# Performance work log

Measured on AMD Instinct MI355X. Metric: run time of the kernel, lower is better.

## Reference

```python
import jax, jax.numpy as jnp
import numpy as np

HEADS = 16
DIM_HEAD = 64
SCALE = DIM_HEAD ** -0.5


def setup_inputs() -> dict:
    key = jax.random.key(0)
    ks = jax.random.split(key, 7)
    b, n, m, d = 2, 2048, 2048, 1024
    inner = HEADS * DIM_HEAD  # 1024
    patch_embed = jax.random.normal(ks[0], (b, n, d), dtype=jnp.float32)
    pixel_embed = jax.random.normal(ks[1], (b, m, d), dtype=jnp.float32)
    s = 1.0 / np.sqrt(d)
    Wq = jax.random.normal(ks[2], (d, inner), dtype=jnp.float32) * s
    Wk = jax.random.normal(ks[3], (d, inner), dtype=jnp.float32) * s
    Wv = jax.random.normal(ks[4], (d, inner), dtype=jnp.float32) * s
    Wo = jax.random.normal(ks[5], (inner, d), dtype=jnp.float32) * (1.0 / np.sqrt(inner))
    bo = jax.random.normal(ks[6], (d,), dtype=jnp.float32) * 0.01
    return {"patch_embed": patch_embed, "pixel_embed": pixel_embed,
            "Wq": Wq, "Wk": Wk, "Wv": Wv, "Wo": Wo, "bo": bo}


def reference(patch_embed, pixel_embed, Wq, Wk, Wv, Wo, bo):
    b, n, _ = patch_embed.shape
    h, dh = HEADS, DIM_HEAD
    # projections
    q = patch_embed @ Wq  # [b, n, h*dh]
    k = pixel_embed @ Wk  # [b, m, h*dh]
    v = pixel_embed @ Wv  # [b, m, h*dh]
    # split heads: [b, seq, h, dh]
    q = q.reshape(b, n, h, dh)
    k = k.reshape(b, -1, h, dh)
    v = v.reshape(b, -1, h, dh)
    sim = jnp.einsum('bihd,bjhd->bhij', q, k) * SCALE  # [b, h, n, m]
    attn = jax.nn.softmax(sim, axis=-1)
    out = jnp.einsum('bhij,bjhd->bihd', attn, v)  # [b, n, h, dh]
    out = out.reshape(b, n, h * dh)
    return out @ Wo + bo  # [b, n, query_dim]
```

## Files before the change

kernel.cpp:

```cpp
#include <hip/hip_runtime.h>

#define SEQ 2048
#define DMODEL 1024
#define HEADS 16
#define DH 64
#define QSCALE 0.180336880f

typedef __attribute__((ext_vector_type(8))) short short8;
typedef __attribute__((ext_vector_type(4))) float f32x4;

__device__ __forceinline__ ushort f2bf(float x) {
  union { float f; unsigned u; } v; v.f = x;
  return (ushort)((v.u + 0x7fffu + ((v.u >> 16) & 1u)) >> 16);
}

__device__ __forceinline__ void gld16(const ushort* g, ushort* l) {
  __builtin_amdgcn_global_load_lds(
      (const __attribute__((address_space(1))) unsigned int*)g,
      (__attribute__((address_space(3))) unsigned int*)l, 16, 0, 0);
}

__device__ __forceinline__ size_t qk_idx(int bh, int s, int d) {
  return ((((size_t)bh * (SEQ / 16) + (s >> 4)) * 2 + (d >> 5)) * 64 +
          ((d >> 3) & 3) * 16 + (s & 15)) * 8 + (d & 7);
}
__device__ __forceinline__ size_t v_idx(int bh, int s, int d) {
  return ((((size_t)bh * 4 + (d >> 4)) * (SEQ / 32) + (s >> 5)) * 64 +
          ((s >> 3) & 3) * 16 + (d & 15)) * 8 + (s & 7);
}

__global__ __launch_bounds__(256) void prologue(
    const float* __restrict__ patch, const float* __restrict__ pixel,
    const float* __restrict__ W0, const float* __restrict__ W1,
    const float* __restrict__ W2, const float* __restrict__ W3,
    ushort* __restrict__ pb, ushort* __restrict__ xb,
    ushort* __restrict__ O0, ushort* __restrict__ O1,
    ushort* __restrict__ O2, ushort* __restrict__ O3) {
  const int z = blockIdx.z;
  const int tx = threadIdx.x, ty = threadIdx.y;
  if (z < 2) {
    const float4* in = (const float4*)(z ? pixel : patch);
    ushort4* out = (ushort4*)(z ? xb : pb);
    const int base = (blockIdx.y * 32 + blockIdx.x) * 256 + ty * 32 + tx;
#pragma unroll
    for (int rep = 0; rep < 4; ++rep) {
      const int i = base + rep * 262144;
      float4 f = in[i];
      out[i] = make_ushort4(f2bf(f.x), f2bf(f.y), f2bf(f.z), f2bf(f.w));
    }
    return;
  }
  __shared__ float tile[32][33];
  const int zz = z - 2;
  const float* in = zz == 0 ? W0 : zz == 1 ? W1 : zz == 2 ? W2 : W3;
  ushort* out = zz == 0 ? O0 : zz == 1 ? O1 : zz == 2 ? O2 : O3;
  const float scale = zz == 0 ? QSCALE : 1.0f;
  const int n0 = blockIdx.x * 32, k0 = blockIdx.y * 32;
#pragma unroll
  for (int i = 0; i < 4; ++i)
    tile[ty + i * 8][tx] = in[(size_t)(k0 + ty + i * 8) * DMODEL + n0 + tx];
  __syncthreads();
#pragma unroll
  for (int i = 0; i < 4; ++i)
    out[(size_t)(n0 + ty + i * 8) * DMODEL + k0 + tx] =
        f2bf(tile[tx][ty + i * 8] * scale);
}

__global__ __launch_bounds__(256) void mfma_gemm_qkv(
    const ushort* __restrict__ pb, const ushort* __restrict__ xb,
    const ushort* __restrict__ wqt, const ushort* __restrict__ wkt,
    const ushort* __restrict__ wvt, ushort* __restrict__ qws,
    ushort* __restrict__ kws, ushort* __restrict__ vws) {
  __shared__ __align__(16) ushort As[128 * 64];
  __shared__ __align__(16) ushort Bs[128 * 64];
  const int z = blockIdx.z;
  const ushort* A = (z == 0) ? pb : xb;
  const ushort* Bt = (z == 0) ? wqt : (z == 1) ? wkt : wvt;

  const int t = threadIdx.x;
  const int w = t >> 6, lane = t & 63, ln = lane & 15, q = lane >> 4;
  const int wm = w & 1, wn = w >> 1;
  const int row0 = blockIdx.y * 128, col0 = blockIdx.x * 128;
  const int sw = ln & 7;

  f32x4 acc[4][4];
#pragma unroll
  for (int i = 0; i < 4; ++i)
#pragma unroll
    for (int j = 0; j < 4; ++j) acc[i][j] = (f32x4){0.f, 0.f, 0.f, 0.f};

  for (int k0 = 0; k0 < DMODEL; k0 += 64) {
    __syncthreads();
#pragma unroll
    for (int rep = 0; rep < 4; ++rep) {
      const int u0 = rep * 256 + w * 64;
      const int u = u0 + lane;
      const int r = u >> 3, gl = (u & 7) ^ (r & 7);
      gld16(&A[(size_t)(row0 + r) * DMODEL + k0 + gl * 8], &As[u0 * 8]);
      gld16(&Bt[(size_t)(col0 + r) * DMODEL + k0 + gl * 8], &Bs[u0 * 8]);
    }
    __syncthreads();
#pragma unroll
    for (int ks = 0; ks < 2; ++ks) {
      short8 af[4], bf[4];
#pragma unroll
      for (int rt = 0; rt < 4; ++rt)
        af[rt] = *(const short8*)&As[(wm * 64 + rt * 16 + ln) * 64 +
                                     (((ks * 4 + q) ^ sw) * 8)];
#pragma unroll
      for (int ct = 0; ct < 4; ++ct)
        bf[ct] = *(const short8*)&Bs[(wn * 64 + ct * 16 + ln) * 64 +
                                     (((ks * 4 + q) ^ sw) * 8)];
#pragma unroll
      for (int rt = 0; rt < 4; ++rt)
#pragma unroll
        for (int ct = 0; ct < 4; ++ct)
          acc[rt][ct] = __builtin_amdgcn_mfma_f32_16x16x32_bf16(af[rt], bf[ct],
                                                                acc[rt][ct], 0, 0, 0);
    }
  }

  if (z < 2) {
    ushort* dst = z == 0 ? qws : kws;
#pragma unroll
    for (int rt = 0; rt < 4; ++rt)
#pragma unroll
      for (int ct = 0; ct < 4; ++ct) {
        const int c = col0 + wn * 64 + ct * 16 + ln;
        const int h = c >> 6, d = c & 63;
#pragma unroll
        for (int reg = 0; reg < 4; ++reg) {
          const int r = row0 + wm * 64 + rt * 16 + q * 4 + reg;
          const int b = r >> 11, s = r & (SEQ - 1);
          dst[qk_idx(b * HEADS + h, s, d)] = f2bf(acc[rt][ct][reg]);
        }
      }
  } else {
#pragma unroll
    for (int rt = 0; rt < 4; ++rt)
#pragma unroll
      for (int ct = 0; ct < 4; ++ct) {
        const int c = col0 + wn * 64 + ct * 16 + ln;
        const int h = c >> 6, d = c & 63;
        const int r0 = row0 + wm * 64 + rt * 16 + q * 4;
        const int b = r0 >> 11, s0 = r0 & (SEQ - 1);
        ushort4 u4 = make_ushort4(f2bf(acc[rt][ct][0]), f2bf(acc[rt][ct][1]),
                                  f2bf(acc[rt][ct][2]), f2bf(acc[rt][ct][3]));
        *(ushort4*)&vws[v_idx(b * HEADS + h, s0, d)] = u4;
      }
  }
}

__global__ __launch_bounds__(256, 3) void flash_mfma(
    const ushort* __restrict__ Qg, const ushort* __restrict__ Kg,
    const ushort* __restrict__ Vg, ushort* __restrict__ Og) {
  __shared__ __align__(16) ushort Kst[2][8 * 512];
  __shared__ __align__(16) ushort Vst[2][8 * 512];
  __shared__ __align__(16) ushort Ps[128 * 72];

  const int t = threadIdx.x;
  const int w = t >> 6, lane = t & 63, ln = lane & 15, q = lane >> 4;
  const int bh = blockIdx.x;
  const int qt = blockIdx.y;

  const ushort* qg = Qg + (size_t)bh * SEQ * DH;
  const ushort* kg = Kg + (size_t)bh * SEQ * DH;
  const ushort* vg = Vg + (size_t)bh * DH * SEQ;

  short8 qf[2][2];
#pragma unroll
  for (int rt = 0; rt < 2; ++rt)
#pragma unroll
    for (int ks = 0; ks < 2; ++ks)
      qf[rt][ks] = *(const short8*)
          &qg[(((size_t)(qt * 8 + w * 2 + rt) * 2 + ks) * 64 + lane) * 8];

  float l_i[2][4];
  f32x4 acc_o[2][4];
#pragma unroll
  for (int rt = 0; rt < 2; ++rt)
#pragma unroll
    for (int reg = 0; reg < 4; ++reg) l_i[rt][reg] = 0.f;
#pragma unroll
  for (int rt = 0; rt < 2; ++rt)
#pragma unroll
    for (int nt = 0; nt < 4; ++nt) acc_o[rt][nt] = (f32x4){0.f, 0.f, 0.f, 0.f};

#pragma unroll
  for (int i = 0; i < 4; ++i) {
    const int f = w * 4 + i;
    if (f < 8) {
      gld16(&kg[(size_t)(0 * 8 + f) * 512 + lane * 8], &Kst[0][f * 512]);
    } else {
      const int f2 = f - 8, nt = f2 >> 1, ks2 = f2 & 1;
      gld16(&vg[(size_t)(nt * (SEQ / 32) + 0 * 2 + ks2) * 512 + lane * 8],
            &Vst[0][f2 * 512]);
    }
  }
  __syncthreads();

  for (int kt = 0; kt < SEQ / 64; ++kt) {
    const int cur = kt & 1;
    if (kt + 1 < SEQ / 64) {
      const int nxt = cur ^ 1;
#pragma unroll
      for (int i = 0; i < 4; ++i) {
        const int f = w * 4 + i;
        if (f < 8) {
          gld16(&kg[(size_t)((kt + 1) * 8 + f) * 512 + lane * 8],
                &Kst[nxt][f * 512]);
        } else {
          const int f2 = f - 8, nt = f2 >> 1, ks2 = f2 & 1;
          gld16(&vg[(size_t)(nt * (SEQ / 32) + (kt + 1) * 2 + ks2) * 512 +
                    lane * 8],
                &Vst[nxt][f2 * 512]);
        }
      }
    }

    f32x4 accs[2][4];
#pragma unroll
    for (int rt = 0; rt < 2; ++rt)
#pragma unroll
      for (int ct = 0; ct < 4; ++ct) accs[rt][ct] = (f32x4){0.f, 0.f, 0.f, 0.f};
#pragma unroll
    for (int ks = 0; ks < 2; ++ks)
#pragma unroll
      for (int ct = 0; ct < 4; ++ct) {
        const short8 bf = *(const short8*)&Kst[cur][(ct * 2 + ks) * 512 + lane * 8];
#pragma unroll
        for (int rt = 0; rt < 2; ++rt)
          accs[rt][ct] = __builtin_amdgcn_mfma_f32_16x16x32_bf16(
              qf[rt][ks], bf, accs[rt][ct], 0, 0, 0);
      }

#pragma unroll
    for (int rt = 0; rt < 2; ++rt)
#pragma unroll
      for (int ct = 0; ct < 4; ++ct)
#pragma unroll
        for (int reg = 0; reg < 4; ++reg) {
          const float p = __builtin_amdgcn_exp2f(accs[rt][ct][reg]);
          l_i[rt][reg] += p;
          union { float f; unsigned u; } v; v.f = p;
          Ps[(w * 32 + rt * 16 + q * 4 + reg) * 72 + ct * 16 + ln] =
              (ushort)((v.u + 0x8000u) >> 16);
        }

#pragma unroll
    for (int ks2 = 0; ks2 < 2; ++ks2) {
      short8 pa[2];
#pragma unroll
      for (int rt = 0; rt < 2; ++rt)
        pa[rt] = *(const short8*)&Ps[(w * 32 + rt * 16 + ln) * 72 +
                                     ks2 * 32 + q * 8];
#pragma unroll
      for (int nt = 0; nt < 4; ++nt) {
        const short8 bv = *(const short8*)&Vst[cur][(nt * 2 + ks2) * 512 + lane * 8];
#pragma unroll
        for (int rt = 0; rt < 2; ++rt)
          acc_o[rt][nt] = __builtin_amdgcn_mfma_f32_16x16x32_bf16(
              pa[rt], bv, acc_o[rt][nt], 0, 0, 0);
      }
    }

    __syncthreads();
  }

  const int b = bh >> 4, h = bh & 15;
#pragma unroll
  for (int rt = 0; rt < 2; ++rt)
#pragma unroll
    for (int reg = 0; reg < 4; ++reg) {
      float l = l_i[rt][reg];
      l += __shfl_xor(l, 1, 16);
      l += __shfl_xor(l, 2, 16);
      l += __shfl_xor(l, 4, 16);
      l += __shfl_xor(l, 8, 16);
      const float inv = 1.0f / l;
      const int s = qt * 128 + w * 32 + rt * 16 + q * 4 + reg;
#pragma unroll
      for (int nt = 0; nt < 4; ++nt)
        Og[(size_t)(b * SEQ + s) * DMODEL + h * DH + nt * 16 + ln] =
            f2bf(acc_o[rt][nt][reg] * inv);
    }
}

__global__ __launch_bounds__(256) void mfma_gemm_out(const ushort* __restrict__ A,
                                                     const ushort* __restrict__ Bt,
                                                     const float* __restrict__ bias,
                                                     float* __restrict__ dst) {
  __shared__ __align__(16) ushort As[64 * 64];
  __shared__ __align__(16) ushort Bs[128 * 64];
  const int t = threadIdx.x;
  const int w = t >> 6, lane = t & 63, ln = lane & 15, q = lane >> 4;
  const int wm = w & 1, wn = w >> 1;
  const int row0 = blockIdx.y * 64, col0 = blockIdx.x * 128;
  const int sw = ln & 7;

  f32x4 acc[2][4];
#pragma unroll
  for (int i = 0; i < 2; ++i)
#pragma unroll
    for (int j = 0; j < 4; ++j) acc[i][j] = (f32x4){0.f, 0.f, 0.f, 0.f};

  for (int k0 = 0; k0 < DMODEL; k0 += 64) {
    __syncthreads();
#pragma unroll
    for (int rep = 0; rep < 2; ++rep) {
      const int u0 = rep * 256 + w * 64;
      const int u = u0 + lane;
      const int r = u >> 3, gl = (u & 7) ^ (r & 7);
      gld16(&A[(size_t)(row0 + r) * DMODEL + k0 + gl * 8], &As[u0 * 8]);
    }
#pragma unroll
    for (int rep = 0; rep < 4; ++rep) {
      const int u0 = rep * 256 + w * 64;
      const int u = u0 + lane;
      const int r = u >> 3, gl = (u & 7) ^ (r & 7);
      gld16(&Bt[(size_t)(col0 + r) * DMODEL + k0 + gl * 8], &Bs[u0 * 8]);
    }
    __syncthreads();
#pragma unroll
    for (int ks = 0; ks < 2; ++ks) {
      short8 af[2], bf[4];
#pragma unroll
      for (int rt = 0; rt < 2; ++rt)
        af[rt] = *(const short8*)&As[(wm * 32 + rt * 16 + ln) * 64 +
                                     (((ks * 4 + q) ^ sw) * 8)];
#pragma unroll
      for (int ct = 0; ct < 4; ++ct)
        bf[ct] = *(const short8*)&Bs[(wn * 64 + ct * 16 + ln) * 64 +
                                     (((ks * 4 + q) ^ sw) * 8)];
#pragma unroll
      for (int rt = 0; rt < 2; ++rt)
#pragma unroll
        for (int ct = 0; ct < 4; ++ct)
          acc[rt][ct] = __builtin_amdgcn_mfma_f32_16x16x32_bf16(af[rt], bf[ct],
                                                                acc[rt][ct], 0, 0, 0);
    }
  }

#pragma unroll
  for (int rt = 0; rt < 2; ++rt)
#pragma unroll
    for (int ct = 0; ct < 4; ++ct) {
      const int c = col0 + wn * 64 + ct * 16 + ln;
      const float bi = bias[c];
#pragma unroll
      for (int reg = 0; reg < 4; ++reg) {
        const int r = row0 + wm * 32 + rt * 16 + q * 4 + reg;
        dst[(size_t)r * DMODEL + c] = acc[rt][ct][reg] + bi;
      }
    }
}

extern "C" void kernel_launch(void* const* d_in, const int* in_sizes, int n_in,
                              void* d_out, int out_size, void* d_ws,
                              size_t ws_size, hipStream_t stream) {
  const float* patch = (const float*)d_in[0];
  const float* pixel = (const float*)d_in[1];
  const float* Wq = (const float*)d_in[2];
  const float* Wk = (const float*)d_in[3];
  const float* Wv = (const float*)d_in[4];
  const float* Wo = (const float*)d_in[5];
  const float* bo = (const float*)d_in[6];
  float* out = (float*)d_out;

  const size_t E = (size_t)2 * SEQ * DMODEL;
  const size_t W = (size_t)DMODEL * DMODEL;
  ushort* pb  = (ushort*)d_ws;
  ushort* xb  = pb + E;
  ushort* wqt = xb + E;
  ushort* wkt = wqt + W;
  ushort* wvt = wkt + W;
  ushort* wot = wvt + W;
  ushort* qws = wot + W;
  ushort* kws = qws + E;
  ushort* vws = kws + E;
  ushort* aws = vws + E;

  prologue<<<dim3(32, 32, 6), dim3(32, 8), 0, stream>>>(
      patch, pixel, Wq, Wk, Wv, Wo, pb, xb, wqt, wkt, wvt, wot);
  mfma_gemm_qkv<<<dim3(8, 32, 3), 256, 0, stream>>>(pb, xb, wqt, wkt, wvt,
                                                    qws, kws, vws);
  flash_mfma<<<dim3(32, 16), 256, 0, stream>>>(qws, kws, vws, aws);
  mfma_gemm_out<<<dim3(8, 64), 256, 0, stream>>>(aws, wot, bo, out);
}
```

Before: 195.9 us.

## Switch P and V to fp16 with packed conversion, merge K/V LDS buffers

Stores V and the softmax probabilities as fp16 using the packed cvt_pkrtz instruction in place of manual bf16 rounding, and runs the PV product with the f16 MFMA. K and V staging buffers are merged into one LDS array with precomputed source pointers and strides, which removes per-iteration index arithmetic. Occupancy hint lowered from 3 to 2 blocks per CU, allowing more registers per thread. fp16 gives more mantissa precision than bf16 but less range; the probabilities are at most about 1 and the V projections are moderate, so overflow is unlikely.

```diff
diff --git a/kernel.cpp b/kernel.cpp
--- a/kernel.cpp
+++ b/kernel.cpp
@@ -8,10 +8,18 @@
 
 typedef __attribute__((ext_vector_type(8))) short short8;
 typedef __attribute__((ext_vector_type(4))) float f32x4;
+typedef _Float16 half8 __attribute__((ext_vector_type(8)));
+typedef __fp16 fp16x2 __attribute__((ext_vector_type(2)));
 
 __device__ __forceinline__ ushort f2bf(float x) {
   union { float f; unsigned u; } v; v.f = x;
   return (ushort)((v.u + 0x7fffu + ((v.u >> 16) & 1u)) >> 16);
+}
+
+__device__ __forceinline__ ushort2 pk16(float x, float y) {
+  union { fp16x2 h; ushort2 u; } v;
+  v.h = __builtin_amdgcn_cvt_pkrtz(x, y);
+  return v.u;
 }
 
 __device__ __forceinline__ void gld16(const ushort* g, ushort* l) {
@@ -144,18 +152,18 @@
         const int h = c >> 6, d = c & 63;
         const int r0 = row0 + wm * 64 + rt * 16 + q * 4;
         const int b = r0 >> 11, s0 = r0 & (SEQ - 1);
-        ushort4 u4 = make_ushort4(f2bf(acc[rt][ct][0]), f2bf(acc[rt][ct][1]),
-                                  f2bf(acc[rt][ct][2]), f2bf(acc[rt][ct][3]));
-        *(ushort4*)&vws[v_idx(b * HEADS + h, s0, d)] = u4;
-      }
-  }
-}
-
-__global__ __launch_bounds__(256, 3) void flash_mfma(
+        const ushort2 p01 = pk16(acc[rt][ct][0], acc[rt][ct][1]);
+        const ushort2 p23 = pk16(acc[rt][ct][2], acc[rt][ct][3]);
+        *(ushort4*)&vws[v_idx(b * HEADS + h, s0, d)] =
+            make_ushort4(p01.x, p01.y, p23.x, p23.y);
+      }
+  }
+}
+
+__global__ __launch_bounds__(256, 2) void flash_mfma(
     const ushort* __restrict__ Qg, const ushort* __restrict__ Kg,
     const ushort* __restrict__ Vg, ushort* __restrict__ Og) {
-  __shared__ __align__(16) ushort Kst[2][8 * 512];
-  __shared__ __align__(16) ushort Vst[2][8 * 512];
+  __shared__ __align__(16) ushort KVst[2][16 * 512];
   __shared__ __align__(16) ushort Ps[128 * 72];
 
   const int t = threadIdx.x;
@@ -167,6 +175,25 @@
   const ushort* kg = Kg + (size_t)bh * SEQ * DH;
   const ushort* vg = Vg + (size_t)bh * DH * SEQ;
 
+  const ushort* sp[4];
+  int sstride[4];
+  ushort* ld0[4];
+  ushort* ld1[4];
+#pragma unroll
+  for (int i = 0; i < 4; ++i) {
+    const int f = w * 4 + i;
+    if (f < 8) {
+      sp[i] = kg + (size_t)f * 512 + lane * 8;
+      sstride[i] = 8 * 512;
+    } else {
+      const int f2 = f - 8, nt = f2 >> 1, ks2 = f2 & 1;
+      sp[i] = vg + ((size_t)nt * (SEQ / 32) + ks2) * 512 + lane * 8;
+      sstride[i] = 2 * 512;
+    }
+    ld0[i] = &KVst[0][f * 512];
+    ld1[i] = &KVst[1][f * 512];
+  }
+
   short8 qf[2][2];
 #pragma unroll
   for (int rt = 0; rt < 2; ++rt)
@@ -188,33 +215,21 @@
 
 #pragma unroll
   for (int i = 0; i < 4; ++i) {
-    const int f = w * 4 + i;
-    if (f < 8) {
-      gld16(&kg[(size_t)(0 * 8 + f) * 512 + lane * 8], &Kst[0][f * 512]);
-    } else {
-      const int f2 = f - 8, nt = f2 >> 1, ks2 = f2 & 1;
-      gld16(&vg[(size_t)(nt * (SEQ / 32) + 0 * 2 + ks2) * 512 + lane * 8],
-            &Vst[0][f2 * 512]);
-    }
+    gld16(sp[i], ld0[i]);
+    sp[i] += sstride[i];
   }
   __syncthreads();
+
+  const int prow = w * 32;
 
   for (int kt = 0; kt < SEQ / 64; ++kt) {
     const int cur = kt & 1;
+    const ushort* KV = KVst[cur];
     if (kt + 1 < SEQ / 64) {
-      const int nxt = cur ^ 1;
 #pragma unroll
       for (int i = 0; i < 4; ++i) {
-        const int f = w * 4 + i;
-        if (f < 8) {
-          gld16(&kg[(size_t)((kt + 1) * 8 + f) * 512 + lane * 8],
-                &Kst[nxt][f * 512]);
-        } else {
-          const int f2 = f - 8, nt = f2 >> 1, ks2 = f2 & 1;
-          gld16(&vg[(size_t)(nt * (SEQ / 32) + (kt + 1) * 2 + ks2) * 512 +
-                    lane * 8],
-                &Vst[nxt][f2 * 512]);
-        }
+        gld16(sp[i], cur ? ld0[i] : ld1[i]);
+        sp[i] += sstride[i];
       }
     }
 
@@ -227,7 +242,7 @@
     for (int ks = 0; ks < 2; ++ks)
 #pragma unroll
       for (int ct = 0; ct < 4; ++ct) {
-        const short8 bf = *(const short8*)&Kst[cur][(ct * 2 + ks) * 512 + lane * 8];
+        const short8 bf = *(const short8*)&KV[(ct * 2 + ks) * 512 + lane * 8];
 #pragma unroll
         for (int rt = 0; rt < 2; ++rt)
           accs[rt][ct] = __builtin_amdgcn_mfma_f32_16x16x32_bf16(
@@ -237,29 +252,35 @@
 #pragma unroll
     for (int rt = 0; rt < 2; ++rt)
 #pragma unroll
-      for (int ct = 0; ct < 4; ++ct)
+      for (int ct = 0; ct < 4; ++ct) {
+        float p[4];
 #pragma unroll
         for (int reg = 0; reg < 4; ++reg) {
-          const float p = __builtin_amdgcn_exp2f(accs[rt][ct][reg]);
-          l_i[rt][reg] += p;
-          union { float f; unsigned u; } v; v.f = p;
-          Ps[(w * 32 + rt * 16 + q * 4 + reg) * 72 + ct * 16 + ln] =
-              (ushort)((v.u + 0x8000u) >> 16);
+          p[reg] = __builtin_amdgcn_exp2f(accs[rt][ct][reg]);
+          l_i[rt][reg] += p[reg];
         }
+        const int col = ct * 16 + ln;
+        const int r0 = prow + rt * 16 + q * 4;
+        const ushort2 p01 = pk16(p[0], p[1]);
+        const ushort2 p23 = pk16(p[2], p[3]);
+        Ps[(r0 + 0) * 72 + col] = p01.x;
+        Ps[(r0 + 1) * 72 + col] = p01.y;
+        Ps[(r0 + 2) * 72 + col] = p23.x;
+        Ps[(r0 + 3) * 72 + col] = p23.y;
+      }
 
 #pragma unroll
     for (int ks2 = 0; ks2 < 2; ++ks2) {
-      short8 pa[2];
+      half8 pa[2];
 #pragma unroll
       for (int rt = 0; rt < 2; ++rt)
-        pa[rt] = *(const short8*)&Ps[(w * 32 + rt * 16 + ln) * 72 +
-                                     ks2 * 32 + q * 8];
+        pa[rt] = *(const half8*)&Ps[(prow + rt * 16 + ln) * 72 + ks2 * 32 + q * 8];
 #pragma unroll
       for (int nt = 0; nt < 4; ++nt) {
-        const short8 bv = *(const short8*)&Vst[cur][(nt * 2 + ks2) * 512 + lane * 8];
+        const half8 bv = *(const half8*)&KV[(8 + nt * 2 + ks2) * 512 + lane * 8];
 #pragma unroll
         for (int rt = 0; rt < 2; ++rt)
-          acc_o[rt][nt] = __builtin_amdgcn_mfma_f32_16x16x32_bf16(
+          acc_o[rt][nt] = __builtin_amdgcn_mfma_f32_16x16x32_f16(
               pa[rt], bv, acc_o[rt][nt], 0, 0, 0);
       }
     }
```

Measured after the change: 212.3 us. +8.4%, slower.
